# Performance work log

Hardware: AMD Instinct MI355X
Metric: run time of the kernel (lower is better)

The kernel has to match this reference:

```python
import math
import jax, jax.numpy as jnp
import numpy as np

B, S, D_MODEL, H = 8, 1024, 512, 8
HEAD = D_MODEL // H
MAX_REL = 16


def rel_index(length_q, length_k):
    # clipped relative-position index matrix [Lq, Lk] in [0, 2*MAX_REL]
    rq = jnp.arange(length_q)
    rk = jnp.arange(length_k)
    dist = rk[None, :] - rq[:, None]
    return jnp.clip(dist, -MAX_REL, MAX_REL) + MAX_REL


def setup_inputs() -> dict:
    key = jax.random.key(0)
    ks = jax.random.split(key, 13)
    sc = 1.0 / math.sqrt(D_MODEL)
    inp = {
        "query": jax.random.normal(ks[0], (B, S, D_MODEL), jnp.float32),
        "key": jax.random.normal(ks[1], (B, S, D_MODEL), jnp.float32),
        "value": jax.random.normal(ks[2], (B, S, D_MODEL), jnp.float32),
        "Wq": jax.random.normal(ks[3], (D_MODEL, D_MODEL), jnp.float32) * sc,
        "bq": jnp.zeros((D_MODEL,), jnp.float32),
        "Wk": jax.random.normal(ks[4], (D_MODEL, D_MODEL), jnp.float32) * sc,
        "bk": jnp.zeros((D_MODEL,), jnp.float32),
        "Wv": jax.random.normal(ks[5], (D_MODEL, D_MODEL), jnp.float32) * sc,
        "bv": jnp.zeros((D_MODEL,), jnp.float32),
        "Wo": jax.random.normal(ks[6], (D_MODEL, D_MODEL), jnp.float32) * sc,
        "bo": jnp.zeros((D_MODEL,), jnp.float32),
        "rel_k_table": jax.random.normal(ks[7], (2 * MAX_REL + 1, HEAD), jnp.float32),
        "rel_v_table": jax.random.normal(ks[8], (2 * MAX_REL + 1, HEAD), jnp.float32),
    }
    return inp


def reference(query, key, value, Wq, bq, Wk, bk, Wv, bv, Wo, bo, rel_k_table, rel_v_table):
    b, s, d = query.shape
    # input projections (torch Linear: x @ W.T + b)
    q = query @ Wq.T + bq  # [B,S,D]
    k = key @ Wk.T + bk
    v = value @ Wv.T + bv
    # split heads: [B,H,S,HEAD]
    qh = q.reshape(b, s, H, HEAD).transpose(0, 2, 1, 3)
    kh = k.reshape(b, s, H, HEAD).transpose(0, 2, 1, 3)
    vh = v.reshape(b, s, H, HEAD).transpose(0, 2, 1, 3)
    # content-content scores
    attn1 = jnp.einsum("bhqd,bhkd->bhqk", qh, kh)
    # content-position scores via gathered relative embeddings [S,S,HEAD]
    idx = rel_index(s, s)
    rk = rel_k_table[idx]
    attn2 = jnp.einsum("bhqd,qkd->bhqk", qh, rk)
    # NOTE: original code scales by sqrt(batch_size), reproduced faithfully
    scale = math.sqrt(float(B))
    attn = jax.nn.softmax((attn1 + attn2) / scale, axis=-1)
    # values: content + relative-position value term
    w1 = jnp.einsum("bhqk,bhkd->bhqd", attn, vh)
    rv = rel_v_table[idx]
    w2 = jnp.einsum("bhqk,qkd->bhqd", attn, rv)
    x = (w1 + w2).transpose(0, 2, 1, 3).reshape(b * s, d)
    return x @ Wo.T + bo
```

## Files before the change

kernel.cpp:

```cpp
#include <hip/hip_runtime.h>

typedef unsigned short u16;
typedef float f32x4 __attribute__((ext_vector_type(4)));
typedef float f32x16 __attribute__((ext_vector_type(16)));
typedef __bf16 bf16x8 __attribute__((ext_vector_type(8)));

#define MFMA16(a, b, c) __builtin_amdgcn_mfma_f32_16x16x32_bf16((a), (b), (c), 0, 0, 0)
#define MFMA32(a, b, c) __builtin_amdgcn_mfma_f32_32x32x16_bf16((a), (b), (c), 0, 0, 0)

#define B_ 8
#define H_ 8
#define S_ 1024

__device__ __forceinline__ u16 f2bf(float f) {
  unsigned u = __float_as_uint(f);
  return (u16)((u + 0x7fffu + ((u >> 16) & 1u)) >> 16);
}
__device__ __forceinline__ unsigned cvtpk(float a, float b) {
  unsigned r;
  asm("v_cvt_pk_bf16_f32 %0, %1, %2" : "=v"(r) : "v"(a), "v"(b));
  return r;
}
__device__ __forceinline__ void plswap(unsigned& a, unsigned& b) {
  asm("v_permlane32_swap_b32 %0, %1" : "+v"(a), "+v"(b));
}
__device__ __forceinline__ void gload16(const void* g, void* l) {
  __builtin_amdgcn_global_load_lds((__attribute__((address_space(1))) const void*)g,
                                   (__attribute__((address_space(3))) void*)l, 16, 0, 0);
}

__global__ void __launch_bounds__(256) convAll(const float* __restrict__ q, const float* __restrict__ k,
                                               const float* __restrict__ v, const float* __restrict__ Wq,
                                               const float* __restrict__ Wk, const float* __restrict__ Wv,
                                               const float* __restrict__ Wo, const float* __restrict__ relk,
                                               u16* __restrict__ dq, u16* __restrict__ dk, u16* __restrict__ dv,
                                               u16* __restrict__ dWq, u16* __restrict__ dWk, u16* __restrict__ dWv,
                                               u16* __restrict__ dWo, u16* __restrict__ drelk) {
  const int bid = blockIdx.x;
  const float* s; u16* d; size_t off;
  if (bid < 12288) {
    size_t i4 = (size_t)bid * 256 + threadIdx.x;
    int tsel = (int)(i4 >> 20);
    off = (i4 & 1048575) << 2;
    s = tsel == 0 ? q : (tsel == 1 ? k : v);
    d = tsel == 0 ? dq : (tsel == 1 ? dk : dv);
  } else {
    size_t i = ((size_t)(bid - 12288) * 256 + threadIdx.x) << 2;
    if (i >= 1050688) return;
    if (i < 262144)       { s = Wq; d = dWq; off = i; }
    else if (i < 524288)  { s = Wk; d = dWk; off = i - 262144; }
    else if (i < 786432)  { s = Wv; d = dWv; off = i - 524288; }
    else if (i < 1048576) { s = Wo; d = dWo; off = i - 786432; }
    else                  { s = relk; d = drelk; off = i - 1048576; }
  }
  float4 f = *(const float4*)(s + off);
  uint2 o;
  o.x = cvtpk(f.x, f.y);
  o.y = cvtpk(f.z, f.w);
  *(uint2*)(d + off) = o;
}

__global__ void __launch_bounds__(256) qkv_gemm(const u16* __restrict__ Xq, const u16* __restrict__ Xk,
                                                const u16* __restrict__ Xv, const u16* __restrict__ Wqb,
                                                const u16* __restrict__ Wkb, const u16* __restrict__ Wvb,
                                                const float* __restrict__ bq, const float* __restrict__ bk,
                                                const float* __restrict__ bv, u16* __restrict__ Qh,
                                                u16* __restrict__ Kh, u16* __restrict__ Vt) {
  __shared__ u16 As[128 * 64];
  __shared__ u16 Bs[128 * 64];
  const int seg = blockIdx.x >> 8, bid = blockIdx.x & 255;
  const u16* A = seg == 0 ? Xq : (seg == 1 ? Xk : Xv);
  const u16* W = seg == 0 ? Wqb : (seg == 1 ? Wkb : Wvb);
  const float* bias = seg == 0 ? bq : (seg == 1 ? bk : bv);
  const int tid = threadIdx.x, lane = tid & 63, wid = tid >> 6;
  const int c = lane & 15, g = lane >> 4;
  const int bm = bid >> 2, bn = bid & 3;
  const int m0 = bm << 7, n0 = bn << 7;
  const int wrow = (wid >> 1) << 6, wcol = (wid & 1) << 6;

  const f32x4 ZF = {0.f, 0.f, 0.f, 0.f};
  f32x4 acc[4][4];
#pragma unroll
  for (int i = 0; i < 4; ++i)
#pragma unroll
    for (int j = 0; j < 4; ++j) acc[i][j] = ZF;

  for (int kt = 0; kt < 512; kt += 64) {
    __syncthreads();
#pragma unroll
    for (int i = 0; i < 4; ++i) {
      int Lb = ((wid << 2) | i) << 10;
      int L = Lb + lane * 16;
      int row = L >> 7;
      int off = (L & 127) ^ ((row & 7) << 4);
      gload16((const char*)A + ((((size_t)(m0 + row)) << 9) + kt) * 2 + off, (char*)As + Lb);
      gload16((const char*)W + ((((size_t)(n0 + row)) << 9) + kt) * 2 + off, (char*)Bs + Lb);
    }
    __syncthreads();
#pragma unroll
    for (int kk = 0; kk < 2; ++kk) {
      bf16x8 af[4], bfr[4];
#pragma unroll
      for (int rt = 0; rt < 4; ++rt) {
        int row = wrow + (rt << 4) + c;
        af[rt] = *(const bf16x8*)((const char*)As + row * 128 + (((kk << 6) | (g << 4)) ^ ((row & 7) << 4)));
      }
#pragma unroll
      for (int ct = 0; ct < 4; ++ct) {
        int row = wcol + (ct << 4) + c;
        bfr[ct] = *(const bf16x8*)((const char*)Bs + row * 128 + (((kk << 6) | (g << 4)) ^ ((row & 7) << 4)));
      }
#pragma unroll
      for (int rt = 0; rt < 4; ++rt)
#pragma unroll
        for (int ct = 0; ct < 4; ++ct) acc[rt][ct] = MFMA16(af[rt], bfr[ct], acc[rt][ct]);
    }
  }

#pragma unroll
  for (int rt = 0; rt < 4; ++rt)
#pragma unroll
    for (int ct = 0; ct < 4; ++ct) {
      int n = n0 + wcol + (ct << 4) + c;
      float bv2 = bias[n];
      if (seg == 2) {
        int b2 = m0 >> 10;
        int sbase = (m0 & 1023) + wrow + (rt << 4) + (g << 2);
        int h2 = n >> 6, d2 = n & 63;
        uint2 o;
        o.x = cvtpk(acc[rt][ct][0] + bv2, acc[rt][ct][1] + bv2);
        o.y = cvtpk(acc[rt][ct][2] + bv2, acc[rt][ct][3] + bv2);
        *(uint2*)(Vt + ((((size_t)((b2 << 3) + h2) << 6) + d2) << 10) + sbase) = o;
      } else {
        u16* out = seg == 0 ? Qh : Kh;
#pragma unroll
        for (int r = 0; r < 4; ++r) {
          int m = m0 + wrow + (rt << 4) + (g << 2) + r;
          int b = m >> 10, s = m & 1023, h = n >> 6, d = n & 63;
          out[(((((size_t)(b * H_ + h)) << 10) + s) << 6) + d] = f2bf(acc[rt][ct][r] + bv2);
        }
      }
    }
}

__global__ void __launch_bounds__(256) gemm_out(const u16* __restrict__ A, const u16* __restrict__ W,
                                                const float* __restrict__ bias, float* __restrict__ out) {
  __shared__ u16 As[128 * 64];
  __shared__ u16 Bs[128 * 64];
  const int tid = threadIdx.x, lane = tid & 63, wid = tid >> 6;
  const int c = lane & 15, g = lane >> 4;
  const int bm = blockIdx.x >> 2, bn = blockIdx.x & 3;
  const int m0 = bm << 7, n0 = bn << 7;
  const int wrow = (wid >> 1) << 6, wcol = (wid & 1) << 6;

  const f32x4 ZF = {0.f, 0.f, 0.f, 0.f};
  f32x4 acc[4][4];
#pragma unroll
  for (int i = 0; i < 4; ++i)
#pragma unroll
    for (int j = 0; j < 4; ++j) acc[i][j] = ZF;

  for (int kt = 0; kt < 512; kt += 64) {
    __syncthreads();
#pragma unroll
    for (int i = 0; i < 4; ++i) {
      int Lb = ((wid << 2) | i) << 10;
      int L = Lb + lane * 16;
      int row = L >> 7;
      int off = (L & 127) ^ ((row & 7) << 4);
      gload16((const char*)A + ((((size_t)(m0 + row)) << 9) + kt) * 2 + off, (char*)As + Lb);
      gload16((const char*)W + ((((size_t)(n0 + row)) << 9) + kt) * 2 + off, (char*)Bs + Lb);
    }
    __syncthreads();
#pragma unroll
    for (int kk = 0; kk < 2; ++kk) {
      bf16x8 af[4], bfr[4];
#pragma unroll
      for (int rt = 0; rt < 4; ++rt) {
        int row = wrow + (rt << 4) + c;
        af[rt] = *(const bf16x8*)((const char*)As + row * 128 + (((kk << 6) | (g << 4)) ^ ((row & 7) << 4)));
      }
#pragma unroll
      for (int ct = 0; ct < 4; ++ct) {
        int row = wcol + (ct << 4) + c;
        bfr[ct] = *(const bf16x8*)((const char*)Bs + row * 128 + (((kk << 6) | (g << 4)) ^ ((row & 7) << 4)));
      }
#pragma unroll
      for (int rt = 0; rt < 4; ++rt)
#pragma unroll
        for (int ct = 0; ct < 4; ++ct) acc[rt][ct] = MFMA16(af[rt], bfr[ct], acc[rt][ct]);
    }
  }

#pragma unroll
  for (int rt = 0; rt < 4; ++rt)
#pragma unroll
    for (int ct = 0; ct < 4; ++ct) {
      int n = n0 + wcol + (ct << 4) + c;
      float bv = bias[n];
#pragma unroll
      for (int r = 0; r < 4; ++r) {
        int m = m0 + wrow + (rt << 4) + (g << 2) + r;
        out[(((size_t)m) << 9) + n] = acc[rt][ct][r] + bv;
      }
    }
}

__global__ void __launch_bounds__(256) flash_kernel(const u16* __restrict__ Qh, const u16* __restrict__ Kh,
                                                    const u16* __restrict__ Vt, const u16* __restrict__ relkb,
                                                    const float* __restrict__ relv, u16* __restrict__ Xout) {
  __shared__ u16 Ks[2][64 * 64];
  __shared__ u16 Vs[2][64 * 64];
  __shared__ float qrelT[33 * 128];
  __shared__ u16 Pband[128 * 32];
  __shared__ float rv32S[64];
  __shared__ float2 normS[128];

  const int tid = threadIdx.x, lane = tid & 63, wid = tid >> 6;
  const int c32 = lane & 31, hi = lane >> 5;
  const int swz = ((blockIdx.x & 7) << 6) | (blockIdx.x >> 3);
  const int bh = swz >> 3, qt = swz & 7;
  const int qbase = qt << 7;
  const size_t rowbase = ((size_t)bh) << 10;
  const int wavebase = wid << 5;
  const int qloc = wavebase + c32;
  const float K1 = 0.51013619f;
  const float C0 = 24.0f;

#define STAGE(buf, kt_) do { \
    const int k64_ = (kt_) << 6; \
    _Pragma("unroll") \
    for (int i_ = 0; i_ < 2; ++i_) { \
      const int f_ = (wid << 1) | i_; \
      gload16((const char*)Kh + ((rowbase + k64_ + ((f_ & 1) << 5) + c32) << 7) + ((f_ >> 1) << 5) + (hi << 4), \
              (char*)Ks[buf] + (f_ << 10)); \
      gload16((const char*)Vt + ((((size_t)(bh << 6)) + ((f_ & 1) << 5) + c32) << 11) + \
                  ((k64_ + ((f_ >> 1) << 4) + (hi << 3)) << 1), \
              (char*)Vs[buf] + (f_ << 10)); \
    } \
  } while (0)

  STAGE(0, 0);

  ((uint4*)Pband)[tid] = uint4{0, 0, 0, 0};
  ((uint4*)Pband)[tid + 256] = uint4{0, 0, 0, 0};
  if (tid < 64) rv32S[tid] = relv[2048 + tid];

  {
    const int c = lane & 15, g = lane >> 4;
    const f32x4 ZF4 = {0.f, 0.f, 0.f, 0.f};
#pragma unroll
    for (int hf = 0; hf < 2; ++hf) {
      const int q16 = wavebase + (hf << 4) + c;
      const u16* qp = Qh + ((rowbase + qbase + q16) << 6);
      bf16x8 qa0 = *(const bf16x8*)(qp + (g << 3));
      bf16x8 qa1 = *(const bf16x8*)(qp + 32 + (g << 3));
#pragma unroll
      for (int t = 0; t < 3; ++t) {
        int rr = t * 16 + c; if (rr > 32) rr = 32;
        f32x4 qr = ZF4;
        qr = MFMA16(*(const bf16x8*)(relkb + (rr << 6) + (g << 3)), qa0, qr);
        qr = MFMA16(*(const bf16x8*)(relkb + (rr << 6) + 32 + (g << 3)), qa1, qr);
#pragma unroll
        for (int j = 0; j < 4; ++j) {
          int r = t * 16 + (g << 2) + j;
          if (r < 33) qrelT[(r << 7) + q16] = qr[j] * K1 - C0;
        }
      }
    }
  }

  bf16x8 qb[4];
  {
    const u16* qp = Qh + ((rowbase + qbase + qloc) << 6);
#pragma unroll
    for (int ks = 0; ks < 4; ++ks) qb[ks] = *(const bf16x8*)(qp + (ks << 4) + (hi << 3));
  }

  __syncthreads();

  const float bias_lo = qrelT[qloc];
  const float bias_hi = qrelT[(32 << 7) + qloc];
  const int lb16 = lane << 4;

  const f32x16 Z16 = {0.f,0.f,0.f,0.f,0.f,0.f,0.f,0.f,0.f,0.f,0.f,0.f,0.f,0.f,0.f,0.f};
  f32x16 acc0 = Z16, acc1 = Z16;
  float lsum = 0.f, lowsum = 0.f, psum = 0.f;

  for (int kt = 0; kt < 16; ++kt) {
    const int cur = kt & 1;
    if (kt < 15) STAGE(cur ^ 1, kt + 1);

    f32x16 sA = Z16, sB = Z16;
#pragma unroll
    for (int ks = 0; ks < 4; ++ks) {
      bf16x8 ka0 = *(const bf16x8*)((const char*)Ks[cur] + (((ks << 1) | 0) << 10) + lb16);
      bf16x8 ka1 = *(const bf16x8*)((const char*)Ks[cur] + (((ks << 1) | 1) << 10) + lb16);
      sA = MFMA32(ka0, qb[ks], sA);
      sB = MFMA32(ka1, qb[ks], sB);
    }

    const int E = (kt << 6) - qbase - wavebase;
    if (E >= 48) {
      float t0 = 0.f;
#pragma unroll
      for (int r = 0; r < 16; ++r) {
        float pe = __builtin_amdgcn_exp2f(fmaf(sA[r], K1, bias_hi)); sA[r] = pe; t0 += pe;
        float pf = __builtin_amdgcn_exp2f(fmaf(sB[r], K1, bias_hi)); sB[r] = pf; t0 += pf;
      }
      lsum += t0;
    } else if (E <= -80) {
      float t0 = 0.f;
#pragma unroll
      for (int r = 0; r < 16; ++r) {
        float pe = __builtin_amdgcn_exp2f(fmaf(sA[r], K1, bias_lo)); sA[r] = pe; t0 += pe;
        float pf = __builtin_amdgcn_exp2f(fmaf(sB[r], K1, bias_lo)); sB[r] = pf; t0 += pf;
      }
      lsum += t0; lowsum += t0;
    } else {
      const int base = E - c32 + (hi << 2);
#pragma unroll
      for (int mt = 0; mt < 2; ++mt) {
        f32x16& s = mt ? sB : sA;
#pragma unroll
        for (int r = 0; r < 16; ++r) {
          int dlt = base + (mt << 5) + (r & 3) + ((r >> 2) << 3);
          int idx = dlt < -16 ? 0 : (dlt > 16 ? 32 : dlt + 16);
          float pe = __builtin_amdgcn_exp2f(fmaf(s[r], K1, qrelT[(idx << 7) + qloc]));
          s[r] = pe;
          lsum += pe;
          if (dlt <= -16) lowsum += pe;
          else if (dlt < 16) { psum += pe; Pband[(qloc << 5) + dlt + 16] = f2bf(pe); }
        }
      }
    }

    unsigned uA[8], uB[8];
#pragma unroll
    for (int j = 0; j < 8; ++j) {
      uA[j] = cvtpk(sA[2 * j], sA[2 * j + 1]);
      uB[j] = cvtpk(sB[2 * j], sB[2 * j + 1]);
    }
    bf16x8 pa[4];
#pragma unroll
    for (int ks = 0; ks < 4; ++ks) {
      int jb = (ks & 1) << 2;
      unsigned w0, w1, w2, w3;
      if (ks < 2) { w0 = uA[jb]; w2 = uA[jb + 2]; w1 = uA[jb + 1]; w3 = uA[jb + 3]; }
      else        { w0 = uB[jb]; w2 = uB[jb + 2]; w1 = uB[jb + 1]; w3 = uB[jb + 3]; }
      plswap(w0, w2);
      plswap(w1, w3);
      uint4 t4{w0, w1, w2, w3};
      pa[ks] = __builtin_bit_cast(bf16x8, t4);
    }

#pragma unroll
    for (int ks = 0; ks < 4; ++ks) {
      bf16x8 vb0 = *(const bf16x8*)((const char*)Vs[cur] + (((ks << 1) | 0) << 10) + lb16);
      bf16x8 vb1 = *(const bf16x8*)((const char*)Vs[cur] + (((ks << 1) | 1) << 10) + lb16);
      acc0 = MFMA32(pa[ks], vb0, acc0);
      acc1 = MFMA32(pa[ks], vb1, acc1);
    }
    __syncthreads();
  }

  lsum += __shfl_xor(lsum, 32);
  lowsum += __shfl_xor(lowsum, 32);
  psum += __shfl_xor(psum, 32);
  const float inv = 1.f / lsum;
  const float hsum = lsum - lowsum - psum;
  if (lane < 32) {
    Pband[qloc << 5] = f2bf(lowsum);
    normS[qloc] = float2{inv, hsum};
  }
  __syncthreads();
  u16* rvT = (u16*)qrelT;
  for (int i = tid; i < 2048; i += 256) rvT[i] = f2bf(relv[((i & 31) << 6) + (i >> 5)]);
  __syncthreads();

#pragma unroll
  for (int ks2 = 0; ks2 < 2; ++ks2) {
    bf16x8 pf = *(const bf16x8*)(Pband + (qloc << 5) + (ks2 << 4) + (hi << 3));
    bf16x8 rv0 = *(const bf16x8*)(rvT + (c32 << 5) + (ks2 << 4) + (hi << 3));
    bf16x8 rv1 = *(const bf16x8*)(rvT + ((32 + c32) << 5) + (ks2 << 4) + (hi << 3));
    acc0 = MFMA32(pf, rv0, acc0);
    acc1 = MFMA32(pf, rv1, acc1);
  }

  const int b = bh >> 3, h = bh & 7;
  const float rvA = rv32S[c32], rvB = rv32S[32 + c32];
#pragma unroll
  for (int r = 0; r < 16; ++r) {
    int qw = wavebase + (r & 3) + ((r >> 2) << 3) + (hi << 2);
    float2 nh = normS[qw];
    size_t orow = ((((size_t)b << 10) + (qbase + qw)) << 9) + (h << 6);
    Xout[orow + c32]      = f2bf((acc0[r] + nh.y * rvA) * nh.x);
    Xout[orow + 32 + c32] = f2bf((acc1[r] + nh.y * rvB) * nh.x);
  }
#undef STAGE
}

extern "C" void kernel_launch(void* const* d_in, const int* in_sizes, int n_in,
                              void* d_out, int out_size, void* d_ws, size_t ws_size,
                              hipStream_t stream) {
  (void)in_sizes; (void)n_in; (void)out_size; (void)ws_size;
  const float* query = (const float*)d_in[0];
  const float* key   = (const float*)d_in[1];
  const float* value = (const float*)d_in[2];
  const float* Wq = (const float*)d_in[3];
  const float* bq = (const float*)d_in[4];
  const float* Wk = (const float*)d_in[5];
  const float* bk = (const float*)d_in[6];
  const float* Wv = (const float*)d_in[7];
  const float* bv = (const float*)d_in[8];
  const float* Wo = (const float*)d_in[9];
  const float* bo = (const float*)d_in[10];
  const float* relk = (const float*)d_in[11];
  const float* relv = (const float*)d_in[12];

  char* ws = (char*)d_ws;
  u16*   Xq    = (u16*)(ws + 0);
  u16*   Xk    = (u16*)(ws + 8388608);
  u16*   Xv    = (u16*)(ws + 16777216);
  u16*   Wqb   = (u16*)(ws + 25165824);
  u16*   Wkb   = (u16*)(ws + 25690112);
  u16*   Wvb   = (u16*)(ws + 26214400);
  u16*   Wob   = (u16*)(ws + 26738688);
  u16*   relkb = (u16*)(ws + 27262976);
  u16*   Qh    = (u16*)(ws + 27271168);
  u16*   Kh    = (u16*)(ws + 35659776);
  u16*   Vt    = (u16*)(ws + 52436992);
  u16*   Xout  = (u16*)(ws + 70262784);

  convAll<<<13315, 256, 0, stream>>>(query, key, value, Wq, Wk, Wv, Wo, relk,
                                     Xq, Xk, Xv, Wqb, Wkb, Wvb, Wob, relkb);
  qkv_gemm<<<768, 256, 0, stream>>>(Xq, Xk, Xv, Wqb, Wkb, Wvb, bq, bk, bv, Qh, Kh, Vt);
  flash_kernel<<<512, 256, 0, stream>>>(Qh, Kh, Vt, relkb, relv, Xout);
  gemm_out<<<256, 256, 0, stream>>>(Xout, Wob, bo, (float*)d_out);
}
```

Baseline: 104.2 us.

## Triple-buffer K/V tiles with explicit vmcnt waits and MFMA priority hints

Replaces the double-buffered K/V staging in the flash attention kernel with a three-deep ring, issuing loads two tiles ahead and using explicit s_waitcnt vmcnt counts with raw barriers instead of __syncthreads. It also raises wave priority around the MFMA blocks and splits the softmax row-sum into four partial accumulators to shorten the dependency chain. The aim is to hide global-load latency better and overlap compute across waves. The cost is more LDS (which may reduce occupancy) and fragile hand-tuned waitcnt counts that assume a fixed number of outstanding loads.

```diff
diff --git a/kernel.cpp b/kernel.cpp
--- a/kernel.cpp
+++ b/kernel.cpp
@@ -209,8 +209,8 @@
 __global__ void __launch_bounds__(256) flash_kernel(const u16* __restrict__ Qh, const u16* __restrict__ Kh,
                                                     const u16* __restrict__ Vt, const u16* __restrict__ relkb,
                                                     const float* __restrict__ relv, u16* __restrict__ Xout) {
-  __shared__ u16 Ks[2][64 * 64];
-  __shared__ u16 Vs[2][64 * 64];
+  __shared__ u16 Ks[3][64 * 64];
+  __shared__ u16 Vs[3][64 * 64];
   __shared__ float qrelT[33 * 128];
   __shared__ u16 Pband[128 * 32];
   __shared__ float rv32S[64];
@@ -227,20 +227,22 @@
   const float K1 = 0.51013619f;
   const float C0 = 24.0f;
 
-#define STAGE(buf, kt_) do { \
+#define STAGE(buf_, kt_) do { \
     const int k64_ = (kt_) << 6; \
     _Pragma("unroll") \
     for (int i_ = 0; i_ < 2; ++i_) { \
       const int f_ = (wid << 1) | i_; \
       gload16((const char*)Kh + ((rowbase + k64_ + ((f_ & 1) << 5) + c32) << 7) + ((f_ >> 1) << 5) + (hi << 4), \
-              (char*)Ks[buf] + (f_ << 10)); \
+              (char*)Ks[buf_] + (f_ << 10)); \
       gload16((const char*)Vt + ((((size_t)(bh << 6)) + ((f_ & 1) << 5) + c32) << 11) + \
                   ((k64_ + ((f_ >> 1) << 4) + (hi << 3)) << 1), \
-              (char*)Vs[buf] + (f_ << 10)); \
+              (char*)Vs[buf_] + (f_ << 10)); \
     } \
   } while (0)
 
   STAGE(0, 0);
+  STAGE(1, 1);
+  STAGE(2, 2);
 
   ((uint4*)Pband)[tid] = uint4{0, 0, 0, 0};
   ((uint4*)Pband)[tid + 256] = uint4{0, 0, 0, 0};
@@ -287,11 +289,10 @@
   f32x16 acc0 = Z16, acc1 = Z16;
   float lsum = 0.f, lowsum = 0.f, psum = 0.f;
 
+  int cur = 0;
   for (int kt = 0; kt < 16; ++kt) {
-    const int cur = kt & 1;
-    if (kt < 15) STAGE(cur ^ 1, kt + 1);
-
     f32x16 sA = Z16, sB = Z16;
+    __builtin_amdgcn_s_setprio(1);
 #pragma unroll
     for (int ks = 0; ks < 4; ++ks) {
       bf16x8 ka0 = *(const bf16x8*)((const char*)Ks[cur] + (((ks << 1) | 0) << 10) + lb16);
@@ -299,23 +300,27 @@
       sA = MFMA32(ka0, qb[ks], sA);
       sB = MFMA32(ka1, qb[ks], sB);
     }
+    __builtin_amdgcn_s_setprio(0);
 
     const int E = (kt << 6) - qbase - wavebase;
     if (E >= 48) {
-      float t0 = 0.f;
+      float ps[4] = {0.f, 0.f, 0.f, 0.f};
 #pragma unroll
       for (int r = 0; r < 16; ++r) {
-        float pe = __builtin_amdgcn_exp2f(fmaf(sA[r], K1, bias_hi)); sA[r] = pe; t0 += pe;
-        float pf = __builtin_amdgcn_exp2f(fmaf(sB[r], K1, bias_hi)); sB[r] = pf; t0 += pf;
-      }
-      lsum += t0;
+        float pe = __builtin_amdgcn_exp2f(fmaf(sA[r], K1, bias_hi)); sA[r] = pe;
+        float pf = __builtin_amdgcn_exp2f(fmaf(sB[r], K1, bias_hi)); sB[r] = pf;
+        ps[r & 3] += pe + pf;
+      }
+      lsum += (ps[0] + ps[1]) + (ps[2] + ps[3]);
     } else if (E <= -80) {
-      float t0 = 0.f;
+      float ps[4] = {0.f, 0.f, 0.f, 0.f};
 #pragma unroll
       for (int r = 0; r < 16; ++r) {
-        float pe = __builtin_amdgcn_exp2f(fmaf(sA[r], K1, bias_lo)); sA[r] = pe; t0 += pe;
-        float pf = __builtin_amdgcn_exp2f(fmaf(sB[r], K1, bias_lo)); sB[r] = pf; t0 += pf;
-      }
+        float pe = __builtin_amdgcn_exp2f(fmaf(sA[r], K1, bias_lo)); sA[r] = pe;
+        float pf = __builtin_amdgcn_exp2f(fmaf(sB[r], K1, bias_lo)); sB[r] = pf;
+        ps[r & 3] += pe + pf;
+      }
+      float t0 = (ps[0] + ps[1]) + (ps[2] + ps[3]);
       lsum += t0; lowsum += t0;
     } else {
       const int base = E - c32 + (hi << 2);
@@ -354,6 +359,7 @@
       pa[ks] = __builtin_bit_cast(bf16x8, t4);
     }
 
+    __builtin_amdgcn_s_setprio(1);
 #pragma unroll
     for (int ks = 0; ks < 4; ++ks) {
       bf16x8 vb0 = *(const bf16x8*)((const char*)Vs[cur] + (((ks << 1) | 0) << 10) + lb16);
@@ -361,7 +367,20 @@
       acc0 = MFMA32(pa[ks], vb0, acc0);
       acc1 = MFMA32(pa[ks], vb1, acc1);
     }
-    __syncthreads();
+    __builtin_amdgcn_s_setprio(0);
+
+    if (kt < 15) {
+      __builtin_amdgcn_s_barrier();
+      __builtin_amdgcn_sched_barrier(0);
+      if (kt < 13) STAGE(cur, kt + 3);
+      if (kt < 13)       asm volatile("s_waitcnt vmcnt(8)" ::: "memory");
+      else if (kt == 13) asm volatile("s_waitcnt vmcnt(4)" ::: "memory");
+      else               asm volatile("s_waitcnt vmcnt(0)" ::: "memory");
+      __builtin_amdgcn_sched_barrier(0);
+      __builtin_amdgcn_s_barrier();
+      __builtin_amdgcn_sched_barrier(0);
+    }
+    cur = (cur == 2) ? 0 : cur + 1;
   }
 
   lsum += __shfl_xor(lsum, 32);
```

Result: slower. 106.6 us (+2.3%).
